# Kernel tuning notes

Measured on AMD Instinct MI355X. Metric: run time of the kernel, lower is better.

Reference implementation:

```python
import jax, jax.numpy as jnp
import numpy as np

B, T, C = 2, 2048, 2048
H = 16
D = C // H  # 128 head dim
EPS = 1.1920929e-07  # torch RMSNorm default eps for fp32 (finfo.eps)
ROPE_BASE = 1000000.0


def setup_inputs() -> dict:
    key = jax.random.key(0)
    k1, k2, k3 = jax.random.split(key, 3)
    x = jax.random.normal(k1, (B, T, C), dtype=jnp.float32)
    w_qkv = jax.random.normal(k2, (C, 3 * C), dtype=jnp.float32) * (C ** -0.5)
    w_proj = jax.random.normal(k3, (C, C), dtype=jnp.float32) * (C ** -0.5)
    q_norm_w = jnp.ones((D,), dtype=jnp.float32)
    k_norm_w = jnp.ones((D,), dtype=jnp.float32)
    return {"x": x, "w_qkv": w_qkv, "w_proj": w_proj,
            "q_norm_w": q_norm_w, "k_norm_w": k_norm_w}


def _rms_norm(x, w):
    var = jnp.mean(jnp.square(x), axis=-1, keepdims=True)
    return x * jax.lax.rsqrt(var + EPS) * w


def _rope_tables(t_len, d_head, dtype):
    inv_freq = 1.0 / (ROPE_BASE ** (jnp.arange(0, d_head, 2, dtype=jnp.float32) / d_head))
    t = jnp.arange(t_len, dtype=jnp.float32)
    freqs = jnp.einsum('i,j->ij', t, inv_freq)          # [T, D/2]
    emb = jnp.concatenate([freqs, freqs], axis=-1)      # [T, D]
    return jnp.cos(emb).astype(dtype), jnp.sin(emb).astype(dtype)


def _rotate_half(x):
    x1, x2 = x[..., : x.shape[-1] // 2], x[..., x.shape[-1] // 2:]
    return jnp.concatenate([-x2, x1], axis=-1)


def reference(x, w_qkv, w_proj, q_norm_w, k_norm_w):
    b, t, c = x.shape
    qkv = x @ w_qkv                                     # [B, T, 3C]
    q, k, v = jnp.split(qkv, 3, axis=-1)
    # [B, H, T, D]
    q = q.reshape(b, t, H, D).transpose(0, 2, 1, 3)
    k = k.reshape(b, t, H, D).transpose(0, 2, 1, 3)
    v = v.reshape(b, t, H, D).transpose(0, 2, 1, 3)
    q = _rms_norm(q, q_norm_w)
    k = _rms_norm(k, k_norm_w)
    cos, sin = _rope_tables(t, D, x.dtype)              # [T, D]
    q = q * cos + _rotate_half(q) * sin
    k = k * cos + _rotate_half(k) * sin
    # NOTE: module uses scale = 1/d_head, not 1/sqrt(d_head)
    scale = 1.0 / D
    att = jnp.einsum('bhqd,bhkd->bhqk', q, k) * scale   # [B, H, T, T]
    causal = jnp.tril(jnp.ones((t, t), dtype=bool))
    att = jnp.where(causal, att, jnp.finfo(att.dtype).min)
    att = jax.nn.softmax(att, axis=-1)
    y = jnp.einsum('bhqk,bhkd->bhqd', att, v)           # [B, H, T, D]
    y = y.transpose(0, 2, 1, 3).reshape(b, t, c)
    return y @ w_proj
```

## Files before the change

kernel.cpp:

```cpp
#include <hip/hip_runtime.h>
#include <stdint.h>

#define Bb   2
#define Tt   2048
#define Cc_  2048
#define Hh   16
#define Dd   128
#define Mm_  4096
#define N1   6144
#define EPSf 1.1920929e-07f
#define SCALE (1.0f/128.0f)

typedef __bf16 bf16;
typedef __attribute__((ext_vector_type(8))) __bf16 bf16x8;
typedef __attribute__((ext_vector_type(4))) float  f32x4;

__device__ __forceinline__ void gl_lds16(const bf16* g, bf16* l) {
  __builtin_amdgcn_global_load_lds(
      (const __attribute__((address_space(1))) unsigned int*)g,
      (__attribute__((address_space(3))) unsigned int*)l, 16, 0, 0);
}

__global__ __launch_bounds__(256) void cvt_bf16(const float* __restrict__ in,
                                                bf16* __restrict__ out, int n) {
  int i = (blockIdx.x * 256 + threadIdx.x) * 4;
  if (i >= n) return;
  float4 v = *(const float4*)(in + i);
  union { bf16 h[4]; uint2 u; } o;
  o.h[0] = (bf16)v.x; o.h[1] = (bf16)v.y; o.h[2] = (bf16)v.z; o.h[3] = (bf16)v.w;
  *(uint2*)(out + i) = o.u;
}

__global__ __launch_bounds__(256) void transpose_cvt(const float* __restrict__ in,
                                                     bf16* __restrict__ out,
                                                     int R, int Cc) {
  __shared__ float tile[64][65];
  int c0 = blockIdx.x * 64, r0 = blockIdx.y * 64;
  int tid = threadIdx.x;
#pragma unroll
  for (int j = 0; j < 16; ++j) {
    int idx = tid + j * 256;
    int r = idx >> 6, c = idx & 63;
    tile[r][c] = in[(size_t)(r0 + r) * Cc + c0 + c];
  }
  __syncthreads();
#pragma unroll
  for (int j = 0; j < 16; ++j) {
    int idx = tid + j * 256;
    int rr = idx & 63, cc = idx >> 6;
    out[(size_t)(c0 + cc) * R + r0 + rr] = (bf16)tile[rr][cc];
  }
}

__global__ __launch_bounds__(256) void vtrans(const bf16* __restrict__ V,
                                              bf16* __restrict__ Vt_) {
  __shared__ bf16 tile[64][72];
  int bh = blockIdx.z, t0 = blockIdx.x * 64, d0 = blockIdx.y * 64;
  int tid = threadIdx.x;
#pragma unroll
  for (int j = 0; j < 2; ++j) {
    int idx = (j * 256 + tid) * 8;
    int r = idx >> 6, c = idx & 63;
    bf16x8 v = *(const bf16x8*)(V + ((size_t)bh * Tt + t0 + r) * Dd + d0 + c);
#pragma unroll
    for (int e = 0; e < 8; ++e) tile[r][c + e] = v[e];
  }
  __syncthreads();
#pragma unroll
  for (int j = 0; j < 2; ++j) {
    int idx = (j * 256 + tid) * 8;
    int dd = idx >> 6, tt = idx & 63;
    bf16x8 v;
#pragma unroll
    for (int e = 0; e < 8; ++e) v[e] = tile[tt + e][dd];
    *(bf16x8*)(Vt_ + ((size_t)bh * Dd + d0 + dd) * Tt + t0 + tt) = v;
  }
}

template <typename OutT>
__global__ __launch_bounds__(256) void gemm_bf16(const bf16* __restrict__ A,
                                                 const bf16* __restrict__ Bt,
                                                 OutT* __restrict__ Cm,
                                                 int Nn, int Kk) {
  __shared__ __align__(16) bf16 As[128 * 64];
  __shared__ __align__(16) bf16 Bs[128 * 64];
  const int tid = threadIdx.x;
  const int wave = tid >> 6, lane = tid & 63;
  const int quad = lane >> 4, li = lane & 15;
  const int wm = wave >> 1, wn = wave & 1;
  const int m0 = blockIdx.y * 128, n0 = blockIdx.x * 128;

  f32x4 acc[4][4] = {};

  for (int kt = 0; kt < Kk; kt += 64) {
    __syncthreads();
#pragma unroll
    for (int j = 0; j < 4; ++j) {
      int c = j * 256 + tid;
      int r = c >> 3, cc = c & 7;
      int gc = ((cc ^ (r & 7)) << 3);
      gl_lds16(A + (size_t)(m0 + r) * Kk + kt + gc, &As[c * 8]);
      gl_lds16(Bt + (size_t)(n0 + r) * Kk + kt + gc, &Bs[c * 8]);
    }
    __syncthreads();
#pragma unroll
    for (int kc = 0; kc < 2; ++kc) {
      bf16x8 af[4], bfr[4];
#pragma unroll
      for (int t = 0; t < 4; ++t) {
        int rowa = wm * 64 + t * 16 + li;
        af[t] = *(const bf16x8*)&As[rowa * 64 + (((kc * 4 + quad) ^ (rowa & 7)) << 3)];
        int rowb = wn * 64 + t * 16 + li;
        bfr[t] = *(const bf16x8*)&Bs[rowb * 64 + (((kc * 4 + quad) ^ (rowb & 7)) << 3)];
      }
#pragma unroll
      for (int mi = 0; mi < 4; ++mi)
#pragma unroll
        for (int ni = 0; ni < 4; ++ni)
          acc[mi][ni] = __builtin_amdgcn_mfma_f32_16x16x32_bf16(af[mi], bfr[ni],
                                                                acc[mi][ni], 0, 0, 0);
    }
  }
#pragma unroll
  for (int mi = 0; mi < 4; ++mi) {
    int row = m0 + wm * 64 + mi * 16 + quad * 4;
#pragma unroll
    for (int ni = 0; ni < 4; ++ni) {
      int col = n0 + wn * 64 + ni * 16 + li;
#pragma unroll
      for (int r = 0; r < 4; ++r)
        Cm[(size_t)(row + r) * Nn + col] = (OutT)acc[mi][ni][r];
    }
  }
}

template <typename OutT>
__global__ __launch_bounds__(512, 2) void gemm256(const bf16* __restrict__ A,
                                                  const bf16* __restrict__ Bt,
                                                  OutT* __restrict__ Cm,
                                                  int Nn, int Kk) {
  __shared__ __align__(16) bf16 As[2][256 * 64];
  __shared__ __align__(16) bf16 Bs[2][128 * 64];
  const int tid = threadIdx.x;
  const int wave = tid >> 6, lane = tid & 63;
  const int quad = lane >> 4, li = lane & 15;
  const int wm = wave >> 2, wn = wave & 3;

  const int nwg = gridDim.x * gridDim.y;
  const int wg  = blockIdx.y * gridDim.x + blockIdx.x;
  const int swz = (wg & 7) * (nwg >> 3) + (wg >> 3);
  const int m0 = (swz / gridDim.x) * 256;
  const int n0 = (swz % gridDim.x) * 128;

  const int NT = Kk >> 6;
  const int lrow = lane >> 3;
  const int lchk = (lane & 7) ^ lrow;

  auto stageA = [&](int tt, int h, int cb) {
    int kt = (tt < NT ? tt : NT - 1) << 6;
#pragma unroll
    for (int j = 0; j < 2; ++j) {
      int seg = j * 8 + wave;
      int r0 = ((seg >> 3) << 7) + (h << 6) + ((seg & 7) << 3);
      gl_lds16(A + (size_t)(m0 + r0 + lrow) * Kk + kt + (lchk << 3),
               &As[cb][r0 * 64]);
    }
  };
  auto stageB = [&](int tt, int cb) {
    int kt = (tt < NT ? tt : NT - 1) << 6;
#pragma unroll
    for (int j = 0; j < 2; ++j) {
      int seg = j * 8 + wave;
      int r0 = seg << 3;
      gl_lds16(Bt + (size_t)(n0 + r0 + lrow) * Kk + kt + (lchk << 3),
               &Bs[cb][r0 * 64]);
    }
  };

  f32x4 acc[8][2] = {};
  bf16x8 afr[4][2], bfr[2][2];

  auto rdA = [&](int h, int cb) {
#pragma unroll
    for (int mi = 0; mi < 4; ++mi) {
      int r = wm * 128 + h * 64 + mi * 16 + li;
#pragma unroll
      for (int kc = 0; kc < 2; ++kc)
        afr[mi][kc] = *(const bf16x8*)&As[cb][r * 64 + (((kc * 4 + quad) ^ (r & 7)) << 3)];
    }
  };
  auto rdB = [&](int cb) {
#pragma unroll
    for (int nj = 0; nj < 2; ++nj) {
      int r = wn * 32 + nj * 16 + li;
#pragma unroll
      for (int kc = 0; kc < 2; ++kc)
        bfr[nj][kc] = *(const bf16x8*)&Bs[cb][r * 64 + (((kc * 4 + quad) ^ (r & 7)) << 3)];
    }
  };
  auto mmac = [&](int mo) {
    __builtin_amdgcn_s_setprio(1);
#pragma unroll
    for (int kc = 0; kc < 2; ++kc)
#pragma unroll
      for (int mi = 0; mi < 4; ++mi)
#pragma unroll
        for (int nj = 0; nj < 2; ++nj)
          acc[mo + mi][nj] = __builtin_amdgcn_mfma_f32_16x16x32_bf16(
              afr[mi][kc], bfr[nj][kc], acc[mo + mi][nj], 0, 0, 0);
    __builtin_amdgcn_s_setprio(0);
  };

  auto tile = [&](int t, int cur, int nxt) {
    rdA(0, cur); rdB(cur);
    stageA(t + 1, 1, nxt);
    asm volatile("s_waitcnt lgkmcnt(8)" ::: "memory");
    __builtin_amdgcn_s_barrier();
    asm volatile("s_waitcnt lgkmcnt(0)" ::: "memory");
    __builtin_amdgcn_sched_barrier(0);
    mmac(0);
    asm volatile("s_waitcnt vmcnt(6)" ::: "memory");
    __builtin_amdgcn_s_barrier();
    rdA(1, cur);
    stageA(t + 2, 0, cur);
    stageB(t + 2, cur);
    __builtin_amdgcn_s_barrier();
    asm volatile("s_waitcnt lgkmcnt(0)" ::: "memory");
    __builtin_amdgcn_sched_barrier(0);
    mmac(4);
    asm volatile("s_waitcnt vmcnt(6)" ::: "memory");
    __builtin_amdgcn_s_barrier();
  };

  stageA(0, 0, 0); stageB(0, 0); stageA(0, 1, 0);
  stageA(1, 0, 1); stageB(1, 1);
  asm volatile("s_waitcnt vmcnt(6)" ::: "memory");
  __builtin_amdgcn_s_barrier();

  for (int t = 0; t < NT; t += 2) {
    tile(t, 0, 1);
    tile(t + 1, 1, 0);
  }
  asm volatile("s_waitcnt vmcnt(0)" ::: "memory");

#pragma unroll
  for (int mi = 0; mi < 8; ++mi) {
    int row = m0 + wm * 128 + mi * 16 + quad * 4;
#pragma unroll
    for (int nj = 0; nj < 2; ++nj) {
      int col = n0 + wn * 32 + nj * 16 + li;
#pragma unroll
      for (int r = 0; r < 4; ++r)
        Cm[(size_t)(row + r) * Nn + col] = (OutT)acc[mi][nj][r];
    }
  }
}

__global__ __launch_bounds__(256) void norm_rope_rearrange(
    const bf16* __restrict__ qkv, const float* __restrict__ qw,
    const float* __restrict__ kw, bf16* __restrict__ Qg,
    bf16* __restrict__ Kg, bf16* __restrict__ Vg) {
  int unit = blockIdx.x * 4 + (threadIdx.x >> 6);
  int lane = threadIdx.x & 63;
  int h = unit & 15;
  int bt = unit >> 4;
  int t = bt & 2047, b = bt >> 11;
  const bf16* base = qkv + (size_t)bt * N1 + h * Dd;
  float q1 = (float)base[lane], q2 = (float)base[lane + 64];
  float k1 = (float)base[Cc_ + lane], k2 = (float)base[Cc_ + lane + 64];
  float v1 = (float)base[2 * Cc_ + lane], v2 = (float)base[2 * Cc_ + lane + 64];
  float sq = q1 * q1 + q2 * q2;
  float sk = k1 * k1 + k2 * k2;
#pragma unroll
  for (int o = 1; o < 64; o <<= 1) { sq += __shfl_xor(sq, o); sk += __shfl_xor(sk, o); }
  float rq = rsqrtf(sq * (1.0f / 128.0f) + EPSf);
  float rk = rsqrtf(sk * (1.0f / 128.0f) + EPSf);
  q1 *= rq * qw[lane]; q2 *= rq * qw[lane + 64];
  k1 *= rk * kw[lane]; k2 *= rk * kw[lane + 64];
  float invf = exp2f((float)lane * (-19.9315685693241740f / 64.0f));
  float ang = (float)t * invf;
  float sn, cs;
  sincosf(ang, &sn, &cs);
  float qo1 = q1 * cs - q2 * sn, qo2 = q2 * cs + q1 * sn;
  float ko1 = k1 * cs - k2 * sn, ko2 = k2 * cs + k1 * sn;
  size_t o1 = ((size_t)(b * Hh + h) * Tt + t) * Dd + lane;
  Qg[o1] = (bf16)qo1; Qg[o1 + 64] = (bf16)qo2;
  Kg[o1] = (bf16)ko1; Kg[o1 + 64] = (bf16)ko2;
  Vg[o1] = (bf16)v1;  Vg[o1 + 64] = (bf16)v2;
}

__global__ __launch_bounds__(256, 3) void attn(const bf16* __restrict__ Qg,
                                               const bf16* __restrict__ Kg,
                                               const bf16* __restrict__ VgT,
                                               bf16* __restrict__ Yg) {
  __shared__ __align__(16) bf16 Kl[64 * 128];
  __shared__ __align__(16) bf16 Vl[128 * 64];
  __shared__ __align__(16) bf16 Pl[4 * 16 * 72];
  const int bh = blockIdx.x;
  const int qt = (int)gridDim.y - 1 - (int)blockIdx.y;
  const int b = bh >> 4, h = bh & 15;
  const int tid = threadIdx.x, wave = tid >> 6, lane = tid & 63;
  const int quad = lane >> 4, li = lane & 15;
  const int q0 = qt * 64;

  const bf16* Qbase = Qg + ((size_t)bh * Tt + q0 + wave * 16 + li) * Dd;
  bf16x8 qf[4];
#pragma unroll
  for (int kc = 0; kc < 4; ++kc) qf[kc] = *(const bf16x8*)(Qbase + kc * 32 + quad * 8);

  f32x4 o[8] = {};
  float L[4] = {};
  bf16* Pw = &Pl[wave * 16 * 72];

  bf16x8 kreg[4];
  auto loadK = [&](int k0) {
#pragma unroll
    for (int j = 0; j < 4; ++j) {
      int c = j * 256 + tid;
      int r = c >> 4, cc = c & 15;
      kreg[j] = *(const bf16x8*)(Kg + ((size_t)bh * Tt + k0 + r) * Dd + ((cc ^ (r & 7)) << 3));
    }
  };
  auto stageV = [&](int k0) {
#pragma unroll
    for (int j = 0; j < 4; ++j) {
      int c = j * 256 + tid;
      int r = c >> 3, cc = c & 7;
      gl_lds16(VgT + ((size_t)bh * Dd + r) * Tt + k0 + ((cc ^ (r & 7)) << 3), &Vl[c * 8]);
    }
  };

  loadK(0);
  stageV(0);

  for (int kt = 0; kt <= qt; ++kt) {
    asm volatile("s_waitcnt vmcnt(4)" ::: "memory");
#pragma unroll
    for (int j = 0; j < 4; ++j) {
      int c = j * 256 + tid;
      *(bf16x8*)&Kl[c * 8] = kreg[j];
    }
    if (kt < qt) loadK(kt * 64 + 64);
    asm volatile("s_waitcnt lgkmcnt(0)" ::: "memory");
    __builtin_amdgcn_s_barrier();
    __builtin_amdgcn_sched_barrier(0);

    f32x4 s4[4] = {};
#pragma unroll
    for (int nt = 0; nt < 4; ++nt) {
      int key = nt * 16 + li;
#pragma unroll
      for (int kc = 0; kc < 4; ++kc) {
        bf16x8 kf = *(const bf16x8*)&Kl[key * 128 + (((kc * 4 + quad) ^ (key & 7)) << 3)];
        s4[nt] = __builtin_amdgcn_mfma_f32_16x16x32_bf16(qf[kc], kf, s4[nt], 0, 0, 0);
      }
    }
    const bool diag = (kt == qt);
#pragma unroll
    for (int nt = 0; nt < 4; ++nt)
#pragma unroll
      for (int r = 0; r < 4; ++r) {
        float e = __expf(s4[nt][r] * SCALE);
        if (diag && (nt * 16 + li > wave * 16 + quad * 4 + r)) e = 0.f;
        L[r] += e;
        Pw[(quad * 4 + r) * 72 + nt * 16 + li] = (bf16)e;
      }
    if (kt < qt) { asm volatile("s_waitcnt vmcnt(4)" ::: "memory"); }
    else         { asm volatile("s_waitcnt vmcnt(0)" ::: "memory"); }
    __builtin_amdgcn_s_barrier();
    __builtin_amdgcn_sched_barrier(0);

#pragma unroll
    for (int kc = 0; kc < 2; ++kc) {
      bf16x8 pf = *(const bf16x8*)&Pw[li * 72 + kc * 32 + quad * 8];
#pragma unroll
      for (int u = 0; u < 8; ++u) {
        bf16x8 vf = *(const bf16x8*)&Vl[(u * 16 + li) * 64 + (((kc * 4 + quad) ^ (li & 7)) << 3)];
        o[u] = __builtin_amdgcn_mfma_f32_16x16x32_bf16(pf, vf, o[u], 0, 0, 0);
      }
    }
    asm volatile("" ::: "memory");
    __builtin_amdgcn_s_barrier();
    __builtin_amdgcn_sched_barrier(0);
    if (kt < qt) stageV(kt * 64 + 64);
  }

  float inv[4];
#pragma unroll
  for (int r = 0; r < 4; ++r) {
    float s0 = L[r];
#pragma unroll
    for (int off = 1; off < 16; off <<= 1) s0 += __shfl_xor(s0, off);
    inv[r] = 1.0f / s0;
  }
  int trow = q0 + wave * 16 + quad * 4;
#pragma unroll
  for (int u = 0; u < 8; ++u) {
    int col = h * Dd + u * 16 + li;
#pragma unroll
    for (int r = 0; r < 4; ++r)
      Yg[(size_t)(b * Tt + trow + r) * Cc_ + col] = (bf16)(o[u][r] * inv[r]);
  }
}

extern "C" void kernel_launch(void* const* d_in, const int* in_sizes, int n_in,
                              void* d_out, int out_size, void* d_ws, size_t ws_size,
                              hipStream_t stream) {
  const float* x      = (const float*)d_in[0];
  const float* w_qkv  = (const float*)d_in[1];
  const float* w_proj = (const float*)d_in[2];
  const float* qnw    = (const float*)d_in[3];
  const float* knw    = (const float*)d_in[4];
  float* out = (float*)d_out;

  bf16* xb     = (bf16*)d_ws;
  bf16* wqkvT  = xb + (size_t)Mm_ * Cc_;
  bf16* wprojT = wqkvT + (size_t)N1 * Cc_;
  bf16* qkv    = wprojT + (size_t)Cc_ * Cc_;
  bf16* Qg     = qkv + (size_t)Mm_ * N1;
  bf16* Kg     = Qg + (size_t)Bb * Hh * Tt * Dd;
  bf16* Vg     = Kg + (size_t)Bb * Hh * Tt * Dd;
  bf16* VgT    = xb;
  bf16* Yg     = qkv;

  hipLaunchKernelGGL(cvt_bf16, dim3((Mm_ * Cc_ / 4) / 256), dim3(256), 0, stream,
                     x, xb, Mm_ * Cc_);
  hipLaunchKernelGGL(transpose_cvt, dim3(N1 / 64, Cc_ / 64), dim3(256), 0, stream,
                     w_qkv, wqkvT, Cc_, N1);
  hipLaunchKernelGGL(transpose_cvt, dim3(Cc_ / 64, Cc_ / 64), dim3(256), 0, stream,
                     w_proj, wprojT, Cc_, Cc_);
  hipLaunchKernelGGL(gemm256<bf16>, dim3(N1 / 128, Mm_ / 256), dim3(512), 0, stream,
                     xb, wqkvT, qkv, N1, Cc_);
  hipLaunchKernelGGL(norm_rope_rearrange, dim3(Bb * Tt * Hh / 4), dim3(256), 0, stream,
                     qkv, qnw, knw, Qg, Kg, Vg);
  hipLaunchKernelGGL(vtrans, dim3(Tt / 64, Dd / 64, Bb * Hh), dim3(256), 0, stream,
                     Vg, VgT);
  hipLaunchKernelGGL(attn, dim3(Bb * Hh, Tt / 64), dim3(256), 0, stream,
                     Qg, Kg, VgT, Yg);
  hipLaunchKernelGGL(gemm256<float>, dim3(Cc_ / 128, Mm_ / 256), dim3(512), 0, stream,
                     Yg, wprojT, out, Cc_, Cc_);
}
```

Before: 376.6 us.

## Fuse RMSNorm, RoPE and V transpose into QKV GEMM epilogue

Replaces the QKV projection GEMM plus the separate norm/rope/rearrange and V-transpose kernels with one 128x128-tile GEMM. Its epilogue stages the tile in LDS and writes normalized, rotated Q/K in head layout, and V already transposed. This removes the round trip of the full qkv intermediate through global memory and two kernel launches. The trade-off is that it swaps the double-buffered 256x128 gemm256 kernel for the simpler single-buffered 128x128 GEMM, which may have lower MFMA throughput. It also adds a serial 32-row per-wave epilogue.

```diff
diff --git a/kernel.cpp b/kernel.cpp
--- a/kernel.cpp
+++ b/kernel.cpp
@@ -52,38 +52,14 @@
   }
 }
 
-__global__ __launch_bounds__(256) void vtrans(const bf16* __restrict__ V,
-                                              bf16* __restrict__ Vt_) {
-  __shared__ bf16 tile[64][72];
-  int bh = blockIdx.z, t0 = blockIdx.x * 64, d0 = blockIdx.y * 64;
-  int tid = threadIdx.x;
-#pragma unroll
-  for (int j = 0; j < 2; ++j) {
-    int idx = (j * 256 + tid) * 8;
-    int r = idx >> 6, c = idx & 63;
-    bf16x8 v = *(const bf16x8*)(V + ((size_t)bh * Tt + t0 + r) * Dd + d0 + c);
-#pragma unroll
-    for (int e = 0; e < 8; ++e) tile[r][c + e] = v[e];
-  }
-  __syncthreads();
-#pragma unroll
-  for (int j = 0; j < 2; ++j) {
-    int idx = (j * 256 + tid) * 8;
-    int dd = idx >> 6, tt = idx & 63;
-    bf16x8 v;
-#pragma unroll
-    for (int e = 0; e < 8; ++e) v[e] = tile[tt + e][dd];
-    *(bf16x8*)(Vt_ + ((size_t)bh * Dd + d0 + dd) * Tt + t0 + tt) = v;
-  }
-}
-
-template <typename OutT>
-__global__ __launch_bounds__(256) void gemm_bf16(const bf16* __restrict__ A,
-                                                 const bf16* __restrict__ Bt,
-                                                 OutT* __restrict__ Cm,
-                                                 int Nn, int Kk) {
-  __shared__ __align__(16) bf16 As[128 * 64];
-  __shared__ __align__(16) bf16 Bs[128 * 64];
+__global__ __launch_bounds__(256) void gemm_qkv_fused(
+    const bf16* __restrict__ A, const bf16* __restrict__ Bt,
+    const float* __restrict__ qw, const float* __restrict__ kw,
+    bf16* __restrict__ Qg, bf16* __restrict__ Kg, bf16* __restrict__ VgT) {
+  __shared__ __align__(16) bf16 smem[128 * 129];
+  bf16* As = smem;
+  bf16* Bs = smem + 128 * 64;
+  const int Kk = Cc_;
   const int tid = threadIdx.x;
   const int wave = tid >> 6, lane = tid & 63;
   const int quad = lane >> 4, li = lane & 15;
@@ -121,15 +97,59 @@
                                                                 acc[mi][ni], 0, 0, 0);
     }
   }
+
+  __syncthreads();
+  bf16 (*tile)[129] = (bf16(*)[129])smem;
 #pragma unroll
   for (int mi = 0; mi < 4; ++mi) {
-    int row = m0 + wm * 64 + mi * 16 + quad * 4;
+    int row = wm * 64 + mi * 16 + quad * 4;
 #pragma unroll
     for (int ni = 0; ni < 4; ++ni) {
-      int col = n0 + wn * 64 + ni * 16 + li;
+      int col = wn * 64 + ni * 16 + li;
 #pragma unroll
       for (int r = 0; r < 4; ++r)
-        Cm[(size_t)(row + r) * Nn + col] = (OutT)acc[mi][ni][r];
+        tile[row + r][col] = (bf16)acc[mi][ni][r];
+    }
+  }
+  __syncthreads();
+
+  const int s = blockIdx.x;
+  const int b = m0 >> 11;
+  const int tloc = m0 & 2047;
+
+  if (s < 32) {
+    const float* w = (s < 16) ? qw : kw;
+    bf16* Og = (s < 16) ? Qg : Kg;
+    const int h = s & 15;
+    const float w1 = w[lane], w2 = w[lane + 64];
+    const float invf = exp2f((float)lane * (-19.9315685693241740f / 64.0f));
+    const size_t hb = (size_t)(b * Hh + h) * Tt;
+    for (int rr = 0; rr < 32; ++rr) {
+      int row = wave * 32 + rr;
+      float x1 = (float)tile[row][lane], x2 = (float)tile[row][lane + 64];
+      float ss = x1 * x1 + x2 * x2;
+#pragma unroll
+      for (int o = 1; o < 64; o <<= 1) ss += __shfl_xor(ss, o);
+      float rn = rsqrtf(ss * (1.0f / 128.0f) + EPSf);
+      x1 *= rn * w1; x2 *= rn * w2;
+      int t = tloc + row;
+      float sn, cs;
+      sincosf((float)t * invf, &sn, &cs);
+      size_t o1 = (hb + t) * Dd + lane;
+      Og[o1]      = (bf16)(x1 * cs - x2 * sn);
+      Og[o1 + 64] = (bf16)(x2 * cs + x1 * sn);
+    }
+  } else {
+    const int h = s - 32;
+    const size_t hb = (size_t)(b * Hh + h) * Dd;
+#pragma unroll
+    for (int it = 0; it < 8; ++it) {
+      int d = it * 16 + (tid >> 4);
+      int t0 = (tid & 15) * 8;
+      bf16x8 v;
+#pragma unroll
+      for (int j = 0; j < 8; ++j) v[j] = tile[t0 + j][d];
+      *(bf16x8*)(VgT + (hb + d) * Tt + tloc + t0) = v;
     }
   }
 }
@@ -254,39 +274,6 @@
         Cm[(size_t)(row + r) * Nn + col] = (OutT)acc[mi][nj][r];
     }
   }
-}
-
-__global__ __launch_bounds__(256) void norm_rope_rearrange(
-    const bf16* __restrict__ qkv, const float* __restrict__ qw,
-    const float* __restrict__ kw, bf16* __restrict__ Qg,
-    bf16* __restrict__ Kg, bf16* __restrict__ Vg) {
-  int unit = blockIdx.x * 4 + (threadIdx.x >> 6);
-  int lane = threadIdx.x & 63;
-  int h = unit & 15;
-  int bt = unit >> 4;
-  int t = bt & 2047, b = bt >> 11;
-  const bf16* base = qkv + (size_t)bt * N1 + h * Dd;
-  float q1 = (float)base[lane], q2 = (float)base[lane + 64];
-  float k1 = (float)base[Cc_ + lane], k2 = (float)base[Cc_ + lane + 64];
-  float v1 = (float)base[2 * Cc_ + lane], v2 = (float)base[2 * Cc_ + lane + 64];
-  float sq = q1 * q1 + q2 * q2;
-  float sk = k1 * k1 + k2 * k2;
-#pragma unroll
-  for (int o = 1; o < 64; o <<= 1) { sq += __shfl_xor(sq, o); sk += __shfl_xor(sk, o); }
-  float rq = rsqrtf(sq * (1.0f / 128.0f) + EPSf);
-  float rk = rsqrtf(sk * (1.0f / 128.0f) + EPSf);
-  q1 *= rq * qw[lane]; q2 *= rq * qw[lane + 64];
-  k1 *= rk * kw[lane]; k2 *= rk * kw[lane + 64];
-  float invf = exp2f((float)lane * (-19.9315685693241740f / 64.0f));
-  float ang = (float)t * invf;
-  float sn, cs;
-  sincosf(ang, &sn, &cs);
-  float qo1 = q1 * cs - q2 * sn, qo2 = q2 * cs + q1 * sn;
-  float ko1 = k1 * cs - k2 * sn, ko2 = k2 * cs + k1 * sn;
-  size_t o1 = ((size_t)(b * Hh + h) * Tt + t) * Dd + lane;
-  Qg[o1] = (bf16)qo1; Qg[o1 + 64] = (bf16)qo2;
-  Kg[o1] = (bf16)ko1; Kg[o1 + 64] = (bf16)ko2;
-  Vg[o1] = (bf16)v1;  Vg[o1 + 64] = (bf16)v2;
 }
 
 __global__ __launch_bounds__(256, 3) void attn(const bf16* __restrict__ Qg,
@@ -416,12 +403,10 @@
   bf16* xb     = (bf16*)d_ws;
   bf16* wqkvT  = xb + (size_t)Mm_ * Cc_;
   bf16* wprojT = wqkvT + (size_t)N1 * Cc_;
-  bf16* qkv    = wprojT + (size_t)Cc_ * Cc_;
-  bf16* Qg     = qkv + (size_t)Mm_ * N1;
+  bf16* Qg     = wprojT + (size_t)Cc_ * Cc_;
   bf16* Kg     = Qg + (size_t)Bb * Hh * Tt * Dd;
-  bf16* Vg     = Kg + (size_t)Bb * Hh * Tt * Dd;
-  bf16* VgT    = xb;
-  bf16* Yg     = qkv;
+  bf16* VgT    = Kg + (size_t)Bb * Hh * Tt * Dd;
+  bf16* Yg     = xb;
 
   hipLaunchKernelGGL(cvt_bf16, dim3((Mm_ * Cc_ / 4) / 256), dim3(256), 0, stream,
                      x, xb, Mm_ * Cc_);
@@ -429,12 +414,8 @@
                      w_qkv, wqkvT, Cc_, N1);
   hipLaunchKernelGGL(transpose_cvt, dim3(Cc_ / 64, Cc_ / 64), dim3(256), 0, stream,
                      w_proj, wprojT, Cc_, Cc_);
-  hipLaunchKernelGGL(gemm256<bf16>, dim3(N1 / 128, Mm_ / 256), dim3(512), 0, stream,
-                     xb, wqkvT, qkv, N1, Cc_);
-  hipLaunchKernelGGL(norm_rope_rearrange, dim3(Bb * Tt * Hh / 4), dim3(256), 0, stream,
-                     qkv, qnw, knw, Qg, Kg, Vg);
-  hipLaunchKernelGGL(vtrans, dim3(Tt / 64, Dd / 64, Bb * Hh), dim3(256), 0, stream,
-                     Vg, VgT);
+  hipLaunchKernelGGL(gemm_qkv_fused, dim3(N1 / 128, Mm_ / 128), dim3(256), 0, stream,
+                     xb, wqkvT, qnw, knw, Qg, Kg, VgT);
   hipLaunchKernelGGL(attn, dim3(Bb * Hh, Tt / 64), dim3(256), 0, stream,
                      Qg, Kg, VgT, Yg);
   hipLaunchKernelGGL(gemm256<float>, dim3(Cc_ / 128, Mm_ / 256), dim3(512), 0, stream,
```

Measured after the change: 392.2 us. 4.1% more time.
